# Performance work log

Hardware: AMD Instinct MI355X
Metric: run time of the kernel (lower is better)

Reference implementation:

```python
import jax, jax.numpy as jnp
import numpy as np

B, T, C, N = 4, 4, 32, 16384
F_OUT = 64
K = 9          # kernel_size
DIL = 1        # dilation
PAD = 4 * DIL  # padding * dilation, as in the torch module


def _unfold1d(a, k, pad, dil):
    """im2col along the last axis. a: [..., N] -> [..., k, N] (stride 1)."""
    ap = jnp.pad(a, [(0, 0)] * (a.ndim - 1) + [(pad, pad)])
    n = a.shape[-1]
    idx = jnp.arange(k)[:, None] * dil + jnp.arange(n)[None, :]  # [k, N]
    return ap[..., idx]


def setup_inputs() -> dict:
    key = jax.random.key(0)
    k1, k2, k3 = jax.random.split(key, 3)
    x = jax.random.normal(k1, (B, T, C, N), dtype=jnp.float32)
    coords = jax.random.normal(k2, (B, T, 3, N), dtype=jnp.float32)
    weight = jax.random.normal(k3, (T, F_OUT, C, K), dtype=jnp.float32) * 0.05
    return {"x": x, "coords": coords, "weight": weight, "sigma": 2}


def reference(x, coords, weight, sigma):
    # im2col windows of features: [B, T, C, K, N]  (channel-major then kernel,
    # matching F.unfold's (C*K, L) layout)
    win = _unfold1d(x, K, PAD, DIL)
    # im2col windows of coords: [B, T, 3, K, N]
    cw = _unfold1d(coords, K, PAD, DIL)
    # subtract center tap (k = K//2)
    diff = cw - cw[:, :, :, K // 2, :][:, :, :, None, :]
    d2 = jnp.sum(diff * diff, axis=2)  # [B, T, K, N]
    # safe sqrt: forward-identical, avoids NaN grads at the zero-distance center
    d = jnp.where(d2 > 0, jnp.sqrt(jnp.where(d2 > 0, d2, 1.0)), 0.0)
    # distance weights, clamped at 0 (torch: dist_weights[dist_weights<0]=0)
    w = jnp.maximum(1.0 - d / sigma, 0.0)  # [B, T, K, N]
    # weight windows; repeat over C in torch == broadcast over C here
    win = win * w[:, :, None, :, :]  # [B, T, C, K, N]
    # batched matmul over flattened (C*K): out[b,t,f,n]
    out = jnp.einsum('btckn,tfck->btfn', win, weight)
    return out
```

## Files before the change

### kernel.cpp

```cpp
#include <hip/hip_runtime.h>
#include <math.h>

#define Bd   4
#define Td   4
#define Cd   32
#define Nd   16384
#define Fd   64
#define Kd   9
#define PADd 4
#define NT   128
#define NROWS (NT + 2*PADd)
#define NCHUNK (NROWS/4)
#define XPITCH 140

typedef __attribute__((ext_vector_type(8))) short  short8;
typedef __attribute__((ext_vector_type(4))) float  float4v;

#define A_WS_BYTES ((size_t)Td * Kd * 4 * 64 * 8 * 2)

__device__ __forceinline__ float sigma_as_float(const void* p) {
    int iv = *(const int*)p;
    if (iv > 0 && iv < 1000000) return (float)iv;
    return __int_as_float(iv);
}

__device__ __forceinline__ unsigned short f32_to_bf16_rne(float v) {
    unsigned int a = __float_as_uint(v);
    a += 0x7fffu + ((a >> 16) & 1u);
    return (unsigned short)(a >> 16);
}

__global__ void prep_weights(const float* __restrict__ w, unsigned short* __restrict__ a) {
    int idx = blockIdx.x * 256 + threadIdx.x;
    if (idx >= Td * Kd * 4 * 64 * 8) return;
    int j    = idx & 7;
    int lane = (idx >> 3) & 63;
    int ft   = (idx >> 9) & 3;
    int k    = (idx >> 11) % Kd;
    int t    = idx / (Kd * 4 * 64 * 8);
    int m = lane & 15, q = lane >> 4;
    int f = ft * 16 + m;
    int c = q * 8 + j;
    float v = w[(((size_t)t * Fd + f) * Cd + c) * Kd + k];
    a[idx] = f32_to_bf16_rne(v);
}

__global__ __launch_bounds__(256, 4)
void swconv_mfma2(const float* __restrict__ x,
                  const float* __restrict__ coords,
                  const unsigned short* __restrict__ aw,
                  const void* __restrict__ sigma_p,
                  float* __restrict__ out)
{
    __shared__ __align__(8) unsigned short xsn[Cd][XPITCH];
    __shared__ float wl[Kd][NT];

    const int tid  = threadIdx.x;
    const int lane = tid & 63;
    const int wv   = tid >> 6;
    const int tile = blockIdx.x, t = blockIdx.y, b = blockIdx.z;
    const int n0   = tile * NT;
    const float inv_sigma = 1.0f / sigma_as_float(sigma_p);

    const float* xbt = x + (size_t)(b * Td + t) * Cd * Nd;
    #pragma unroll 2
    for (int i = tid; i < Cd * NCHUNK; i += 256) {
        int c  = i / NCHUNK;
        int rq = i - c * NCHUNK;
        int nf = n0 - PADd + rq * 4;
        float4 v = make_float4(0.f, 0.f, 0.f, 0.f);
        if (nf >= 0 && nf < Nd)
            v = *reinterpret_cast<const float4*>(xbt + (size_t)c * Nd + nf);
        ushort4 u;
        u.x = f32_to_bf16_rne(v.x);
        u.y = f32_to_bf16_rne(v.y);
        u.z = f32_to_bf16_rne(v.z);
        u.w = f32_to_bf16_rne(v.w);
        *reinterpret_cast<ushort4*>(&xsn[c][rq * 4]) = u;
    }

    {
        const float* cbt = coords + (size_t)(b * Td + t) * 3 * Nd;
        int ln   = tid & (NT - 1);
        int half = tid >> 7;
        int n    = n0 + ln;
        float c0 = cbt[n], c1 = cbt[Nd + n], c2 = cbt[2 * Nd + n];
        int k0 = half ? 5 : 0, k1 = half ? Kd : 5;
        for (int k = k0; k < k1; ++k) {
            int nn = n + k - PADd;
            float d0, d1, d2;
            if (nn >= 0 && nn < Nd) {
                d0 = cbt[nn] - c0; d1 = cbt[Nd + nn] - c1; d2 = cbt[2 * Nd + nn] - c2;
            } else {
                d0 = -c0; d1 = -c1; d2 = -c2;
            }
            float s = d0 * d0 + d1 * d1 + d2 * d2;
            float d = (s > 0.0f) ? sqrtf(s) : 0.0f;
            wl[k][ln] = fmaxf(1.0f - d * inv_sigma, 0.0f);
        }
    }
    __syncthreads();

    const int m = lane & 15, q = lane >> 4;
    const unsigned short* Abase = aw + (size_t)t * Kd * 4 * 64 * 8 + (size_t)lane * 8;

    float4v acc[4][2];
    #pragma unroll
    for (int ft = 0; ft < 4; ++ft)
        #pragma unroll
        for (int nt = 0; nt < 2; ++nt)
            acc[ft][nt] = (float4v){0.f, 0.f, 0.f, 0.f};

    const float4v zero4 = {0.f, 0.f, 0.f, 0.f};

    short8 afr[2][4];
    #pragma unroll
    for (int ft = 0; ft < 4; ++ft)
        afr[0][ft] = *reinterpret_cast<const short8*>(Abase + (size_t)ft * 512);

    for (int k = 0; k < Kd; ++k) {
        const int cur = k & 1;
        if (k + 1 < Kd) {
            #pragma unroll
            for (int ft = 0; ft < 4; ++ft)
                afr[cur ^ 1][ft] = *reinterpret_cast<const short8*>(Abase + (size_t)((k + 1) * 4 + ft) * 512);
        }
        #pragma unroll
        for (int nt = 0; nt < 2; ++nt) {
            const int ncol = wv * 32 + nt * 16 + m;
            const int r    = ncol + k;
            const unsigned short* bp = &xsn[q * 8][r];
            unsigned int p0 = (unsigned int)bp[0]          | ((unsigned int)bp[XPITCH]     << 16);
            unsigned int p1 = (unsigned int)bp[2 * XPITCH] | ((unsigned int)bp[3 * XPITCH] << 16);
            unsigned int p2 = (unsigned int)bp[4 * XPITCH] | ((unsigned int)bp[5 * XPITCH] << 16);
            unsigned int p3 = (unsigned int)bp[6 * XPITCH] | ((unsigned int)bp[7 * XPITCH] << 16);
            uint4 pk = {p0, p1, p2, p3};
            short8 bfr = *reinterpret_cast<short8*>(&pk);
            const float wgt = wl[k][ncol];
            #pragma unroll
            for (int ft = 0; ft < 4; ++ft) {
                float4v d = __builtin_amdgcn_mfma_f32_16x16x32_bf16(afr[cur][ft], bfr, zero4, 0, 0, 0);
                acc[ft][nt][0] = fmaf(wgt, d[0], acc[ft][nt][0]);
                acc[ft][nt][1] = fmaf(wgt, d[1], acc[ft][nt][1]);
                acc[ft][nt][2] = fmaf(wgt, d[2], acc[ft][nt][2]);
                acc[ft][nt][3] = fmaf(wgt, d[3], acc[ft][nt][3]);
            }
        }
    }

    float* ob = out + (size_t)(b * Td + t) * Fd * Nd + n0;
    #pragma unroll
    for (int ft = 0; ft < 4; ++ft) {
        #pragma unroll
        for (int nt = 0; nt < 2; ++nt) {
            const int ncol = wv * 32 + nt * 16 + m;
            #pragma unroll
            for (int rr = 0; rr < 4; ++rr) {
                int f = ft * 16 + q * 4 + rr;
                ob[(size_t)f * Nd + ncol] = acc[ft][nt][rr];
            }
        }
    }
}

__global__ __launch_bounds__(256, 4)
void swconv_f32_kernel(const float* __restrict__ x,
                       const float* __restrict__ coords,
                       const float* __restrict__ weight,
                       const void*  __restrict__ sigma_p,
                       float* __restrict__ out)
{
    __shared__ float xsf[Cd][NROWS + 1];
    __shared__ float csf[3][NROWS + 1];
    const int tid = threadIdx.x;
    const int tile = blockIdx.x, t = blockIdx.y, b = blockIdx.z;
    const int n0 = tile * NT;
    const float inv_sigma = 1.0f / sigma_as_float(sigma_p);

    const float* xbt = x + (size_t)(b * Td + t) * Cd * Nd;
    for (int idx = tid; idx < Cd * NROWS; idx += 256) {
        int c = idx / NROWS, i = idx - c * NROWS, n = n0 - PADd + i;
        xsf[c][i] = (n >= 0 && n < Nd) ? xbt[(size_t)c * Nd + n] : 0.0f;
    }
    const float* cbt = coords + (size_t)(b * Td + t) * 3 * Nd;
    for (int idx = tid; idx < 3 * NROWS; idx += 256) {
        int c = idx / NROWS, i = idx - c * NROWS, n = n0 - PADd + i;
        csf[c][i] = (n >= 0 && n < Nd) ? cbt[(size_t)c * Nd + n] : 0.0f;
    }
    __syncthreads();
    if (tid >= NT) return;

    float wk[Kd];
    {
        const float c0 = csf[0][tid + PADd], c1 = csf[1][tid + PADd], c2 = csf[2][tid + PADd];
        #pragma unroll
        for (int k = 0; k < Kd; ++k) {
            float d0 = csf[0][tid + k] - c0, d1 = csf[1][tid + k] - c1, d2 = csf[2][tid + k] - c2;
            float s = d0 * d0 + d1 * d1 + d2 * d2;
            float d = (s > 0.0f) ? sqrtf(s) : 0.0f;
            wk[k] = fmaxf(1.0f - d * inv_sigma, 0.0f);
        }
    }
    float accf[Fd];
    #pragma unroll
    for (int f = 0; f < Fd; ++f) accf[f] = 0.0f;
    const float* wt = weight + (size_t)t * Fd * Cd * Kd;
    for (int c = 0; c < Cd; ++c) {
        float xv[Kd];
        #pragma unroll
        for (int k = 0; k < Kd; ++k) xv[k] = xsf[c][tid + k];
        const float* wp = wt + c * Kd;
        #pragma unroll
        for (int k = 0; k < Kd; ++k) {
            float v = xv[k] * wk[k];
            #pragma unroll
            for (int f = 0; f < Fd; ++f)
                accf[f] = fmaf(v, wp[(size_t)f * Cd * Kd + k], accf[f]);
        }
    }
    float* op = out + (size_t)(b * Td + t) * Fd * Nd + n0 + tid;
    #pragma unroll
    for (int f = 0; f < Fd; ++f) op[(size_t)f * Nd] = accf[f];
}

extern "C" void kernel_launch(void* const* d_in, const int* in_sizes, int n_in,
                              void* d_out, int out_size, void* d_ws, size_t ws_size,
                              hipStream_t stream) {
    const float* x      = (const float*)d_in[0];
    const float* coords = (const float*)d_in[1];
    const float* weight = (const float*)d_in[2];
    const void*  sigma  = d_in[3];
    float* out = (float*)d_out;

    if (ws_size >= A_WS_BYTES) {
        unsigned short* aw = (unsigned short*)d_ws;
        prep_weights<<<(Td * Kd * 4 * 64 * 8 + 255) / 256, 256, 0, stream>>>(weight, aw);
        dim3 grid(Nd / NT, Td, Bd);
        swconv_mfma2<<<grid, dim3(256), 0, stream>>>(x, coords, aw, sigma, out);
    } else {
        dim3 grid(Nd / NT, Td, Bd);
        swconv_f32_kernel<<<grid, dim3(256), 0, stream>>>(x, coords, weight, sigma, out);
    }
}
```

Baseline: 132.5 us.

## Stage coords in LDS, make distance weights wave-local, and vectorize output stores via LDS

```diff
diff --git a/kernel.cpp b/kernel.cpp
--- a/kernel.cpp
+++ b/kernel.cpp
@@ -12,11 +12,17 @@
 #define NROWS (NT + 2*PADd)
 #define NCHUNK (NROWS/4)
 #define XPITCH 140
+#define EPIT 36
 
 typedef __attribute__((ext_vector_type(8))) short  short8;
 typedef __attribute__((ext_vector_type(4))) float  float4v;
 
 #define A_WS_BYTES ((size_t)Td * Kd * 4 * 64 * 8 * 2)
+
+#define SM_XSN 0
+#define SM_WL  8960
+#define SM_CS  13568
+#define SM_BYTES 18432
 
 __device__ __forceinline__ float sigma_as_float(const void* p) {
     int iv = *(const int*)p;
@@ -46,14 +52,16 @@
 }
 
 __global__ __launch_bounds__(256, 4)
-void swconv_mfma2(const float* __restrict__ x,
+void swconv_mfma3(const float* __restrict__ x,
                   const float* __restrict__ coords,
                   const unsigned short* __restrict__ aw,
                   const void* __restrict__ sigma_p,
                   float* __restrict__ out)
 {
-    __shared__ __align__(8) unsigned short xsn[Cd][XPITCH];
-    __shared__ float wl[Kd][NT];
+    __shared__ __align__(16) unsigned char smem[SM_BYTES];
+    unsigned short (*xsn)[XPITCH] = (unsigned short (*)[XPITCH])(smem + SM_XSN);
+    float (*wl)[NT]               = (float (*)[NT])(smem + SM_WL);
+    float (*cs)[NROWS]            = (float (*)[NROWS])(smem + SM_CS);
 
     const int tid  = threadIdx.x;
     const int lane = tid & 63;
@@ -79,30 +87,38 @@
         *reinterpret_cast<ushort4*>(&xsn[c][rq * 4]) = u;
     }
 
+    const float* cbt = coords + (size_t)(b * Td + t) * 3 * Nd;
+    for (int i = tid; i < 3 * NROWS; i += 256) {
+        int c = i / NROWS, r = i - c * NROWS;
+        int n = n0 - PADd + r;
+        cs[c][r] = (n >= 0 && n < Nd) ? cbt[(size_t)c * Nd + n] : 0.0f;
+    }
+
+    const int m = lane & 15, q = lane >> 4;
+    const unsigned short* Abase = aw + (size_t)t * Kd * 4 * 64 * 8 + (size_t)lane * 8;
+    short8 afr[2][4];
+    #pragma unroll
+    for (int ft = 0; ft < 4; ++ft)
+        afr[0][ft] = *reinterpret_cast<const short8*>(Abase + (size_t)ft * 512);
+
+    __syncthreads();
+
     {
-        const float* cbt = coords + (size_t)(b * Td + t) * 3 * Nd;
-        int ln   = tid & (NT - 1);
-        int half = tid >> 7;
-        int n    = n0 + ln;
-        float c0 = cbt[n], c1 = cbt[Nd + n], c2 = cbt[2 * Nd + n];
+        int nl   = wv * 32 + (lane & 31);
+        int half = lane >> 5;
+        int il   = nl + PADd;
+        float c0 = cs[0][il], c1 = cs[1][il], c2 = cs[2][il];
         int k0 = half ? 5 : 0, k1 = half ? Kd : 5;
+        #pragma unroll
         for (int k = k0; k < k1; ++k) {
-            int nn = n + k - PADd;
-            float d0, d1, d2;
-            if (nn >= 0 && nn < Nd) {
-                d0 = cbt[nn] - c0; d1 = cbt[Nd + nn] - c1; d2 = cbt[2 * Nd + nn] - c2;
-            } else {
-                d0 = -c0; d1 = -c1; d2 = -c2;
-            }
+            float d0 = cs[0][nl + k] - c0;
+            float d1 = cs[1][nl + k] - c1;
+            float d2 = cs[2][nl + k] - c2;
             float s = d0 * d0 + d1 * d1 + d2 * d2;
             float d = (s > 0.0f) ? sqrtf(s) : 0.0f;
-            wl[k][ln] = fmaxf(1.0f - d * inv_sigma, 0.0f);
-        }
-    }
-    __syncthreads();
-
-    const int m = lane & 15, q = lane >> 4;
-    const unsigned short* Abase = aw + (size_t)t * Kd * 4 * 64 * 8 + (size_t)lane * 8;
+            wl[k][nl] = fmaxf(1.0f - d * inv_sigma, 0.0f);
+        }
+    }
 
     float4v acc[4][2];
     #pragma unroll
@@ -110,13 +126,7 @@
         #pragma unroll
         for (int nt = 0; nt < 2; ++nt)
             acc[ft][nt] = (float4v){0.f, 0.f, 0.f, 0.f};
-
     const float4v zero4 = {0.f, 0.f, 0.f, 0.f};
-
-    short8 afr[2][4];
-    #pragma unroll
-    for (int ft = 0; ft < 4; ++ft)
-        afr[0][ft] = *reinterpret_cast<const short8*>(Abase + (size_t)ft * 512);
 
     for (int k = 0; k < Kd; ++k) {
         const int cur = k & 1;
@@ -148,17 +158,29 @@
         }
     }
 
-    float* ob = out + (size_t)(b * Td + t) * Fd * Nd + n0;
-    #pragma unroll
-    for (int ft = 0; ft < 4; ++ft) {
-        #pragma unroll
-        for (int nt = 0; nt < 2; ++nt) {
-            const int ncol = wv * 32 + nt * 16 + m;
-            #pragma unroll
-            for (int rr = 0; rr < 4; ++rr) {
-                int f = ft * 16 + q * 4 + rr;
-                ob[(size_t)f * Nd + ncol] = acc[ft][nt][rr];
+    __syncthreads();
+    float (*epi)[EPIT] = (float (*)[EPIT])(smem + (size_t)wv * 32 * EPIT * 4);
+
+    float* ob = out + (size_t)(b * Td + t) * Fd * Nd + n0 + wv * 32;
+    #pragma unroll
+    for (int fc = 0; fc < 2; ++fc) {
+        #pragma unroll
+        for (int ft2 = 0; ft2 < 2; ++ft2) {
+            const int ft = fc * 2 + ft2;
+            #pragma unroll
+            for (int nt = 0; nt < 2; ++nt) {
+                const int np = nt * 16 + m;
+                #pragma unroll
+                for (int rr = 0; rr < 4; ++rr)
+                    epi[ft2 * 16 + q * 4 + rr][np] = acc[ft][nt][rr];
             }
+        }
+        #pragma unroll
+        for (int inst = 0; inst < 4; ++inst) {
+            const int fl = inst * 8 + (lane >> 3);
+            const int np = (lane & 7) * 4;
+            float4 v = *reinterpret_cast<const float4*>(&epi[fl][np]);
+            *reinterpret_cast<float4*>(ob + (size_t)(fc * 32 + fl) * Nd + np) = v;
         }
     }
 }
@@ -236,7 +258,7 @@
         unsigned short* aw = (unsigned short*)d_ws;
         prep_weights<<<(Td * Kd * 4 * 64 * 8 + 255) / 256, 256, 0, stream>>>(weight, aw);
         dim3 grid(Nd / NT, Td, Bd);
-        swconv_mfma2<<<grid, dim3(256), 0, stream>>>(x, coords, aw, sigma, out);
+        swconv_mfma3<<<grid, dim3(256), 0, stream>>>(x, coords, aw, sigma, out);
     } else {
         dim3 grid(Nd / NT, Td, Bd);
         swconv_f32_kernel<<<grid, dim3(256), 0, stream>>>(x, coords, weight, sigma, out);
```

Result: no change. 130.0 us (-1.9%).
